# Kernel tuning notes

Measured on AMD Instinct MI355X. Metric: run time of the kernel, lower is better.

The kernel has to match this reference:

```python
import jax, jax.numpy as jnp
import numpy as np

NEG_SLOPE = 0.01  # torch F.leaky_relu default


def _mlp_block(x, mask, W, b):
    # x: [B,P,V,F]; mask: [B,P,V] bool; W: [H,F]; b: [H]
    h = jax.nn.leaky_relu(jnp.einsum('bpvf,hf->bpvh', x, W) + b, NEG_SLOPE)
    m = mask[..., None]
    out = jnp.where(m, h, 0.0)                                   # zeros at masked-out slots
    neg = jnp.where(m, out, -jnp.inf)
    pool = jnp.max(neg, axis=2, keepdims=True)                   # [B,P,1,H] masked max-pool
    any_valid = jnp.any(mask, axis=2)[:, :, None, None]
    pool = jnp.where(any_valid, pool, 0.0)                       # fully-masked polylines -> 0
    rep = jnp.broadcast_to(pool, out.shape)
    return jnp.concatenate([out, rep], axis=-1)                  # [B,P,V,2H]


def setup_inputs() -> dict:
    key = jax.random.key(0)
    ks = jax.random.split(key, 8)
    B, P, V, F, H = 32, 512, 32, 16, 64
    input_var = jax.random.normal(ks[0], (B, P, V, F), dtype=jnp.float32)
    input_mask = jax.random.bernoulli(ks[1], 0.8, (B, P, V))
    s = 1.0 / np.sqrt(F)
    W1 = jax.random.uniform(ks[2], (H, F), jnp.float32, -s, s)
    b1 = jax.random.uniform(ks[3], (H,), jnp.float32, -s, s)
    s2 = 1.0 / np.sqrt(2 * H)
    W2 = jax.random.uniform(ks[4], (H, 2 * H), jnp.float32, -s2, s2)
    b2 = jax.random.uniform(ks[5], (H,), jnp.float32, -s2, s2)
    W3 = jax.random.uniform(ks[6], (H, 2 * H), jnp.float32, -s2, s2)
    b3 = jax.random.uniform(ks[7], (H,), jnp.float32, -s2, s2)
    return {"input_var": input_var, "input_mask": input_mask,
            "W1": W1, "b1": b1, "W2": W2, "b2": b2, "W3": W3, "b3": b3,
            "size1": P, "size2": V}


def reference(input_var, input_mask, W1, b1, W2, b2, W3, b3, size1, size2):
    hidden = W1.shape[0]
    x = _mlp_block(input_var, input_mask, W1, b1)
    y = _mlp_block(x, input_mask, W2, b2)
    z = _mlp_block(y, input_mask, W3, b3)
    out = z[:, :, 0, -hidden:]                                   # pooled half, same across V
    out = jnp.where(jnp.any(input_mask, axis=2)[..., None], out, 0.0)
    return out
```

## Files before the change

### kernel.cpp

```cpp
#include <hip/hip_runtime.h>
#include <math.h>

namespace {
constexpr int kXS = 72;
constexpr float kSlope = 0.01f;

typedef short bf16x8 __attribute__((ext_vector_type(8)));
typedef float f32x4  __attribute__((ext_vector_type(4)));

__device__ __forceinline__ float lrelu(float x) { return fmaxf(x, kSlope * x); }

__device__ __forceinline__ unsigned short bfrne(float a) {
    union { float f; unsigned u; } v; v.f = a;
    return (unsigned short)((v.u + 0x7FFFu + ((v.u >> 16) & 1u)) >> 16);
}

__global__ void prep_weights(const float* __restrict__ W1,
                             const float* __restrict__ W2,
                             const float* __restrict__ W3,
                             unsigned short* __restrict__ ws)
{
    int t = blockIdx.x * blockDim.x + threadIdx.x;
    if (t >= 36 * 64) return;
    int f = t >> 6, l = t & 63, c = l & 15, q = l >> 4;
    unsigned short v[8] = {0, 0, 0, 0, 0, 0, 0, 0};
    const float* src = nullptr; int row = 0, k0 = 0, K = 0;
    if (f < 4) {
        if (q < 2) { src = W1; row = 16 * f + c; k0 = q * 8; K = 16; }
    } else if (f < 20) {
        int g = f - 4;  src = W2; row = 16 * (g >> 2) + c; k0 = (g & 3) * 32 + q * 8; K = 128;
    } else {
        int g = f - 20; src = W3; row = 16 * (g >> 2) + c; k0 = (g & 3) * 32 + q * 8; K = 128;
    }
    if (src) {
        #pragma unroll
        for (int j = 0; j < 8; ++j) v[j] = bfrne(src[row * K + k0 + j]);
    }
    unsigned short* dst = ws + (size_t)f * 512 + l * 8;
    *(ushort4*)(dst)     = make_ushort4(v[0], v[1], v[2], v[3]);
    *(ushort4*)(dst + 4) = make_ushort4(v[4], v[5], v[6], v[7]);
}

__global__ __launch_bounds__(256, 4) void fused_mlp_v5(
    const float* __restrict__ X, const int* __restrict__ M,
    const unsigned short* __restrict__ WF,
    const float* __restrict__ B1, const float* __restrict__ B2,
    const float* __restrict__ B3, float* __restrict__ OUT)
{
    __shared__ __align__(16) short sX[4][2][32 * kXS];
    __shared__ __align__(16) short sP[4][2][64];

    const int t = threadIdx.x, w = t >> 6, l = t & 63, c = l & 15, q = l >> 4;
    const size_t bp = (size_t)blockIdx.x * 4 + w;

    short* xb2 = &sX[w][0][0]; short* pl2 = &sP[w][0][0];
    short* xb3 = &sX[w][1][0]; short* pl3 = &sP[w][1][0];

    float4 xr[2][2];
    if (q < 2) {
        #pragma unroll
        for (int mt = 0; mt < 2; ++mt) {
            const float4* p = (const float4*)(X + (bp * 32 + 16 * mt + c) * 16 + q * 8);
            xr[mt][0] = p[0]; xr[mt][1] = p[1];
        }
    }
    const int4* Mp = (const int4*)(M + bp * 32);
    const int4 mr0 = Mp[q], mr1 = Mp[4 + q];
    const unsigned mbits =
        (mr0.x ? 1u : 0u)  | (mr0.y ? 2u : 0u)  | (mr0.z ? 4u : 0u)  | (mr0.w ? 8u : 0u) |
        (mr1.x ? 16u : 0u) | (mr1.y ? 32u : 0u) | (mr1.z ? 64u : 0u) | (mr1.w ? 128u : 0u);
    const bool anyv = __any(mbits != 0);

    float bias1[4], bias2[4], bias3[4];
    #pragma unroll
    for (int nt = 0; nt < 4; ++nt) {
        bias1[nt] = B1[16 * nt + c];
        bias2[nt] = B2[16 * nt + c];
        bias3[nt] = B3[16 * nt + c];
    }

    f32x4 acc[2][4];

    {
        bf16x8 a1f[2];
        #pragma unroll
        for (int mt = 0; mt < 2; ++mt) {
            bf16x8 v = {};
            if (q < 2) {
                float4 f0 = xr[mt][0], f1 = xr[mt][1];
                v[0] = (short)bfrne(f0.x); v[1] = (short)bfrne(f0.y);
                v[2] = (short)bfrne(f0.z); v[3] = (short)bfrne(f0.w);
                v[4] = (short)bfrne(f1.x); v[5] = (short)bfrne(f1.y);
                v[6] = (short)bfrne(f1.z); v[7] = (short)bfrne(f1.w);
            }
            a1f[mt] = v;
        }
        #pragma unroll
        for (int nt = 0; nt < 4; ++nt) {
            bf16x8 wf = *(const bf16x8*)(WF + (size_t)nt * 512 + l * 8);
            f32x4 c0 = { bias1[nt], bias1[nt], bias1[nt], bias1[nt] };
            acc[0][nt] = __builtin_amdgcn_mfma_f32_16x16x32_bf16(a1f[0], wf, c0, 0, 0, 0);
            acc[1][nt] = __builtin_amdgcn_mfma_f32_16x16x32_bf16(a1f[1], wf, c0, 0, 0, 0);
        }
    }

    auto epilogue = [&](short* xb, short* pl) {
        float pool[4];
        #pragma unroll
        for (int nt = 0; nt < 4; ++nt) {
            float pv = -INFINITY;
            #pragma unroll
            for (int mt = 0; mt < 2; ++mt) {
                short* base = &xb[(16 * mt + 4 * q) * kXS + 16 * nt + c];
                #pragma unroll
                for (int r = 0; r < 4; ++r) {
                    float y = lrelu(acc[mt][nt][r]);
                    bool mk = (mbits >> (mt * 4 + r)) & 1;
                    float o = mk ? y : 0.f;
                    pv = mk ? fmaxf(pv, y) : pv;
                    base[r * kXS] = (short)bfrne(o);
                }
            }
            pv = fmaxf(pv, __shfl_xor(pv, 16));
            pv = fmaxf(pv, __shfl_xor(pv, 32));
            pool[nt] = anyv ? pv : 0.f;
        }
        float ps = (q & 2) ? ((q & 1) ? pool[3] : pool[2])
                           : ((q & 1) ? pool[1] : pool[0]);
        pl[16 * q + c] = (short)bfrne(ps);
    };

    auto layerK = [&](const short* xb, const short* pl, int fb, const float (&bias)[4]) {
        bf16x8 a00 = *(const bf16x8*)&xb[(     c) * kXS      + q * 8];
        bf16x8 a01 = *(const bf16x8*)&xb[(16 + c) * kXS      + q * 8];
        bf16x8 a10 = *(const bf16x8*)&xb[(     c) * kXS + 32 + q * 8];
        bf16x8 a11 = *(const bf16x8*)&xb[(16 + c) * kXS + 32 + q * 8];
        bf16x8 ap0 = *(const bf16x8*)&pl[q * 8];
        bf16x8 ap1 = *(const bf16x8*)&pl[32 + q * 8];
        #pragma unroll
        for (int nt = 0; nt < 4; ++nt) {
            acc[0][nt] = f32x4{ bias[nt], bias[nt], bias[nt], bias[nt] };
            acc[1][nt] = acc[0][nt];
        }
        #pragma unroll
        for (int ks = 0; ks < 4; ++ks) {
            bf16x8 am0 = (ks == 0) ? a00 : (ks == 1) ? a10 : (ks == 2) ? ap0 : ap1;
            bf16x8 am1 = (ks == 0) ? a01 : (ks == 1) ? a11 : (ks == 2) ? ap0 : ap1;
            #pragma unroll
            for (int nt = 0; nt < 4; ++nt) {
                bf16x8 wf = *(const bf16x8*)(WF + ((size_t)(fb + nt * 4 + ks)) * 512 + l * 8);
                acc[0][nt] = __builtin_amdgcn_mfma_f32_16x16x32_bf16(am0, wf, acc[0][nt], 0, 0, 0);
                acc[1][nt] = __builtin_amdgcn_mfma_f32_16x16x32_bf16(am1, wf, acc[1][nt], 0, 0, 0);
            }
        }
    };

    epilogue(xb2, pl2);
    layerK(xb2, pl2, 4, bias2);
    epilogue(xb3, pl3);
    layerK(xb3, pl3, 20, bias3);

    {
        float pool[4];
        #pragma unroll
        for (int nt = 0; nt < 4; ++nt) {
            float pv = -INFINITY;
            #pragma unroll
            for (int mt = 0; mt < 2; ++mt)
                #pragma unroll
                for (int r = 0; r < 4; ++r) {
                    bool mk = (mbits >> (mt * 4 + r)) & 1;
                    float y = lrelu(acc[mt][nt][r]);
                    pv = mk ? fmaxf(pv, y) : pv;
                }
            pv = fmaxf(pv, __shfl_xor(pv, 16));
            pv = fmaxf(pv, __shfl_xor(pv, 32));
            pool[nt] = anyv ? pv : 0.f;
        }
        float ps = (q & 2) ? ((q & 1) ? pool[3] : pool[2])
                           : ((q & 1) ? pool[1] : pool[0]);
        OUT[bp * 64 + 16 * q + c] = ps;
    }
}
}

extern "C" void kernel_launch(void* const* d_in, const int* in_sizes, int n_in,
                              void* d_out, int out_size, void* d_ws, size_t ws_size,
                              hipStream_t stream) {
    (void)in_sizes; (void)n_in; (void)ws_size; (void)out_size;
    const float* X  = (const float*)d_in[0];
    const int*   M  = (const int*)d_in[1];
    const float* W1 = (const float*)d_in[2];
    const float* B1 = (const float*)d_in[3];
    const float* W2 = (const float*)d_in[4];
    const float* B2 = (const float*)d_in[5];
    const float* W3 = (const float*)d_in[6];
    const float* B3 = (const float*)d_in[7];
    float* OUT = (float*)d_out;
    unsigned short* WF = (unsigned short*)d_ws;

    prep_weights<<<(36 * 64 + 255) / 256, 256, 0, stream>>>(W1, W2, W3, WF);
    fused_mlp_v5<<<4096, 256, 0, stream>>>(X, M, WF, B1, B2, B3, OUT);
}
```

Measured before the change: 116.6 us.

## Rewrite fused MLP with fp16 32x32 MFMA, packed-half epilogue, and prepacked mask

Replaces the bf16 16x16x32 MFMA path with fp16 32x32x16 MFMA, and each wave now handles two polylines. The epilogue applies bias after the matmul and does leaky-relu and masked max-pool with packed half-precision instructions, using additive -inf mask offsets. Activations go to shared memory in a swizzled byte layout and are regathered with perm. A prep kernel packs the mask into bitfields and converts the weights to fp16. The goal is fewer instructions per element and better MFMA efficiency, at the cost of fp16 rounding in the epilogue and lower occupancy (launch bounds 3).

```diff
diff --git a/kernel.cpp b/kernel.cpp
--- a/kernel.cpp
+++ b/kernel.cpp
@@ -2,185 +2,195 @@
 #include <math.h>
 
 namespace {
-constexpr int kXS = 72;
-constexpr float kSlope = 0.01f;
-
-typedef short bf16x8 __attribute__((ext_vector_type(8)));
-typedef float f32x4  __attribute__((ext_vector_type(4)));
-
-__device__ __forceinline__ float lrelu(float x) { return fmaxf(x, kSlope * x); }
-
-__device__ __forceinline__ unsigned short bfrne(float a) {
-    union { float f; unsigned u; } v; v.f = a;
-    return (unsigned short)((v.u + 0x7FFFu + ((v.u >> 16) & 1u)) >> 16);
-}
-
-__global__ void prep_weights(const float* __restrict__ W1,
-                             const float* __restrict__ W2,
-                             const float* __restrict__ W3,
-                             unsigned short* __restrict__ ws)
+
+typedef _Float16 f16x8 __attribute__((ext_vector_type(8)));
+typedef _Float16 f16x2 __attribute__((ext_vector_type(2)));
+typedef float    f32x16 __attribute__((ext_vector_type(16)));
+typedef unsigned int uint;
+
+__device__ __forceinline__ uint pkrtz(float a, float b) {
+    return __builtin_bit_cast(uint, __builtin_amdgcn_cvt_pkrtz(a, b));
+}
+__device__ __forceinline__ uint pk_add(uint a, uint b) {
+    uint r; asm("v_pk_add_f16 %0, %1, %2" : "=v"(r) : "v"(a), "v"(b)); return r;
+}
+__device__ __forceinline__ uint pk_mul(uint a, uint b) {
+    uint r; asm("v_pk_mul_f16 %0, %1, %2" : "=v"(r) : "v"(a), "v"(b)); return r;
+}
+__device__ __forceinline__ uint pk_max(uint a, uint b) {
+    uint r; asm("v_pk_max_f16 %0, %1, %2" : "=v"(r) : "v"(a), "v"(b)); return r;
+}
+
+__global__ void prep_pack(const float* __restrict__ W1, const float* __restrict__ W2,
+                          const float* __restrict__ W3, const int* __restrict__ M,
+                          unsigned short* __restrict__ wsW, uint* __restrict__ wsM)
 {
     int t = blockIdx.x * blockDim.x + threadIdx.x;
-    if (t >= 36 * 64) return;
-    int f = t >> 6, l = t & 63, c = l & 15, q = l >> 4;
-    unsigned short v[8] = {0, 0, 0, 0, 0, 0, 0, 0};
-    const float* src = nullptr; int row = 0, k0 = 0, K = 0;
-    if (f < 4) {
-        if (q < 2) { src = W1; row = 16 * f + c; k0 = q * 8; K = 16; }
-    } else if (f < 20) {
-        int g = f - 4;  src = W2; row = 16 * (g >> 2) + c; k0 = (g & 3) * 32 + q * 8; K = 128;
-    } else {
-        int g = f - 20; src = W3; row = 16 * (g >> 2) + c; k0 = (g & 3) * 32 + q * 8; K = 128;
-    }
-    if (src) {
-        #pragma unroll
-        for (int j = 0; j < 8; ++j) v[j] = bfrne(src[row * K + k0 + j]);
-    }
-    unsigned short* dst = ws + (size_t)f * 512 + l * 8;
-    *(ushort4*)(dst)     = make_ushort4(v[0], v[1], v[2], v[3]);
-    *(ushort4*)(dst + 4) = make_ushort4(v[4], v[5], v[6], v[7]);
-}
-
-__global__ __launch_bounds__(256, 4) void fused_mlp_v5(
-    const float* __restrict__ X, const int* __restrict__ M,
+    if (t < 34 * 64) {
+        int f = t >> 6, l = t & 63, nb = l & 31, kg = l >> 5;
+        const float* src; int K, ki, nt2;
+        if (f < 2)       { src = W1; K = 16;  ki = 0;           nt2 = f; }
+        else if (f < 18) { int g = f - 2;  src = W2; K = 128; ki = g >> 1; nt2 = g & 1; }
+        else             { int g = f - 18; src = W3; K = 128; ki = g >> 1; nt2 = g & 1; }
+        const float* s = src + (size_t)(32 * nt2 + nb) * K + 16 * ki + 8 * kg;
+        uint4 q;
+        q.x = pkrtz(s[0], s[1]); q.y = pkrtz(s[2], s[3]);
+        q.z = pkrtz(s[4], s[5]); q.w = pkrtz(s[6], s[7]);
+        *(uint4*)(wsW + (size_t)f * 512 + l * 8) = q;
+    } else if (t < 34 * 64 + 16384) {
+        int bp = t - 34 * 64;
+        const int4* mp = (const int4*)(M + bp * 32);
+        uint bits = 0;
+        #pragma unroll
+        for (int i = 0; i < 8; ++i) {
+            int4 v = mp[i];
+            bits |= ((v.x ? 1u : 0u) | (v.y ? 2u : 0u) |
+                     (v.z ? 4u : 0u) | (v.w ? 8u : 0u)) << (4 * i);
+        }
+        wsM[bp] = bits;
+    }
+}
+
+__global__ __launch_bounds__(256, 3) void fused_mlp_v10(
+    const float* __restrict__ X, const uint* __restrict__ MPK,
     const unsigned short* __restrict__ WF,
     const float* __restrict__ B1, const float* __restrict__ B2,
     const float* __restrict__ B3, float* __restrict__ OUT)
 {
-    __shared__ __align__(16) short sX[4][2][32 * kXS];
-    __shared__ __align__(16) short sP[4][2][64];
-
-    const int t = threadIdx.x, w = t >> 6, l = t & 63, c = l & 15, q = l >> 4;
-    const size_t bp = (size_t)blockIdx.x * 4 + w;
-
-    short* xb2 = &sX[w][0][0]; short* pl2 = &sP[w][0][0];
-    short* xb3 = &sX[w][1][0]; short* pl3 = &sP[w][1][0];
-
-    float4 xr[2][2];
-    if (q < 2) {
-        #pragma unroll
-        for (int mt = 0; mt < 2; ++mt) {
-            const float4* p = (const float4*)(X + (bp * 32 + 16 * mt + c) * 16 + q * 8);
-            xr[mt][0] = p[0]; xr[mt][1] = p[1];
-        }
-    }
-    const int4* Mp = (const int4*)(M + bp * 32);
-    const int4 mr0 = Mp[q], mr1 = Mp[4 + q];
-    const unsigned mbits =
-        (mr0.x ? 1u : 0u)  | (mr0.y ? 2u : 0u)  | (mr0.z ? 4u : 0u)  | (mr0.w ? 8u : 0u) |
-        (mr1.x ? 16u : 0u) | (mr1.y ? 32u : 0u) | (mr1.z ? 64u : 0u) | (mr1.w ? 128u : 0u);
-    const bool anyv = __any(mbits != 0);
-
-    float bias1[4], bias2[4], bias3[4];
+    __shared__ __align__(16) unsigned char sXb[4][2][4096];
+    __shared__ __align__(16) _Float16 sP[4][2][64];
+
+    const int t = threadIdx.x, w = t >> 6, l = t & 63;
+    const int hb = l >> 5, mtl = (l >> 4) & 1;
+    const size_t bp0 = (size_t)blockIdx.x * 8 + w * 2;
+
+    unsigned char* sb[2] = { &sXb[w][0][0], &sXb[w][1][0] };
+    _Float16*     pl[2] = { &sP[w][0][0],  &sP[w][1][0]  };
+
+    uint wb0 = (uint)((l & 7) * 32 + mtl * 256 + ((l >> 3) & 1) * 1024 + hb * 8);
+    wb0 ^= (uint)(mtl << 5);
+    const uint wb1 = (wb0 + 512u) ^ 64u;
+    const uint rb = (uint)(mtl * 2048 + hb * 1024 + ((l & 15) >> 1) * 4);
+    const uint sel = (l & 1) ? 0x07060302u : 0x05040100u;
+    const uint SL2 = pkrtz(0.01f, 0.01f);
+
+    bool anyv[2]; uint adm[2][4][2];
     #pragma unroll
-    for (int nt = 0; nt < 4; ++nt) {
-        bias1[nt] = B1[16 * nt + c];
-        bias2[nt] = B2[16 * nt + c];
-        bias3[nt] = B3[16 * nt + c];
-    }
-
-    f32x4 acc[2][4];
+    for (int u = 0; u < 2; ++u) {
+        uint mk = MPK[bp0 + u];
+        anyv[u] = (mk != 0u);
+        #pragma unroll
+        for (int g = 0; g < 4; ++g) {
+            uint nib = (mk >> (8 * g + 4 * hb)) & 15u;
+            adm[u][g][0] = (nib & 1u ? 0u : 0xFC00u) | (nib & 2u ? 0u : 0xFC000000u);
+            adm[u][g][1] = (nib & 4u ? 0u : 0xFC00u) | (nib & 8u ? 0u : 0xFC000000u);
+        }
+    }
+
+    f16x8 a1f[2];
+    #pragma unroll
+    for (int u = 0; u < 2; ++u) {
+        const float4* xp = (const float4*)(X + ((bp0 + u) * 32 + (l & 31)) * 16 + 8 * hb);
+        float4 x0 = xp[0], x1 = xp[1];
+        uint4 q;
+        q.x = pkrtz(x0.x, x0.y); q.y = pkrtz(x0.z, x0.w);
+        q.z = pkrtz(x1.x, x1.y); q.w = pkrtz(x1.z, x1.w);
+        a1f[u] = __builtin_bit_cast(f16x8, q);
+    }
+
+    f32x16 zc;
+    #pragma unroll
+    for (int i = 0; i < 16; ++i) zc[i] = 0.f;
+
+    f32x16 acc[2][2];
 
     {
-        bf16x8 a1f[2];
-        #pragma unroll
-        for (int mt = 0; mt < 2; ++mt) {
-            bf16x8 v = {};
-            if (q < 2) {
-                float4 f0 = xr[mt][0], f1 = xr[mt][1];
-                v[0] = (short)bfrne(f0.x); v[1] = (short)bfrne(f0.y);
-                v[2] = (short)bfrne(f0.z); v[3] = (short)bfrne(f0.w);
-                v[4] = (short)bfrne(f1.x); v[5] = (short)bfrne(f1.y);
-                v[6] = (short)bfrne(f1.z); v[7] = (short)bfrne(f1.w);
+        const _Float16* wp = (const _Float16*)WF + l * 8;
+        f16x8 wf0 = *(const f16x8*)wp;
+        f16x8 wf1 = *(const f16x8*)(wp + 512);
+        #pragma unroll
+        for (int u = 0; u < 2; ++u) {
+            acc[u][0] = __builtin_amdgcn_mfma_f32_32x32x16_f16(a1f[u], wf0, zc, 0, 0, 0);
+            acc[u][1] = __builtin_amdgcn_mfma_f32_32x32x16_f16(a1f[u], wf1, zc, 0, 0, 0);
+        }
+    }
+
+    auto epi = [&](int u, const float* __restrict__ Bp, bool dostore) {
+        unsigned char* sbu = sb[u];
+        _Float16* plu = pl[u];
+        #pragma unroll
+        for (int nt2 = 0; nt2 < 2; ++nt2) {
+            float bsc = Bp[32 * nt2 + (l & 31)];
+            uint bpk = pkrtz(bsc, bsc);
+            uint base = nt2 ? wb1 : wb0;
+            uint pp = 0xFC00FC00u;
+            #pragma unroll
+            for (int g = 0; g < 4; ++g) {
+                uint d01 = pkrtz(acc[u][nt2][4 * g + 0], acc[u][nt2][4 * g + 1]);
+                uint d23 = pkrtz(acc[u][nt2][4 * g + 2], acc[u][nt2][4 * g + 3]);
+                d01 = pk_add(d01, bpk);  d23 = pk_add(d23, bpk);
+                d01 = pk_max(d01, pk_mul(d01, SL2));
+                d23 = pk_max(d23, pk_mul(d23, SL2));
+                if (dostore) {
+                    uint2 st; st.x = d01; st.y = d23;
+                    *(uint2*)(sbu + base + (g >> 1) * 2048 + (g & 1) * 16) = st;
+                }
+                pp = pk_max(pp, pk_add(d01, adm[u][g][0]));
+                pp = pk_max(pp, pk_add(d23, adm[u][g][1]));
             }
-            a1f[mt] = v;
-        }
-        #pragma unroll
-        for (int nt = 0; nt < 4; ++nt) {
-            bf16x8 wf = *(const bf16x8*)(WF + (size_t)nt * 512 + l * 8);
-            f32x4 c0 = { bias1[nt], bias1[nt], bias1[nt], bias1[nt] };
-            acc[0][nt] = __builtin_amdgcn_mfma_f32_16x16x32_bf16(a1f[0], wf, c0, 0, 0, 0);
-            acc[1][nt] = __builtin_amdgcn_mfma_f32_16x16x32_bf16(a1f[1], wf, c0, 0, 0, 0);
-        }
-    }
-
-    auto epilogue = [&](short* xb, short* pl) {
-        float pool[4];
-        #pragma unroll
-        for (int nt = 0; nt < 4; ++nt) {
-            float pv = -INFINITY;
+            f16x2 ph = __builtin_bit_cast(f16x2, pp);
+            float pv = fmaxf((float)ph[0], (float)ph[1]);
+            pv = fmaxf(pv, __shfl_xor(pv, 32));
+            pv = anyv[u] ? pv : 0.f;
+            if (dostore) {
+                if (l < 32) plu[32 * nt2 + (l & 31)] = (_Float16)pv;
+            } else {
+                if (l < 32) OUT[(bp0 + u) * 64 + 32 * nt2 + (l & 31)] = pv;
+            }
+        }
+    };
+
+    auto layerK = [&](int fb) {
+        #pragma unroll
+        for (int ki = 0; ki < 8; ++ki) {
+            const _Float16* wp = (const _Float16*)WF + (size_t)(fb + 2 * ki) * 512 + l * 8;
+            f16x8 wf0 = *(const f16x8*)wp;
+            f16x8 wf1 = *(const f16x8*)(wp + 512);
             #pragma unroll
-            for (int mt = 0; mt < 2; ++mt) {
-                short* base = &xb[(16 * mt + 4 * q) * kXS + 16 * nt + c];
-                #pragma unroll
-                for (int r = 0; r < 4; ++r) {
-                    float y = lrelu(acc[mt][nt][r]);
-                    bool mk = (mbits >> (mt * 4 + r)) & 1;
-                    float o = mk ? y : 0.f;
-                    pv = mk ? fmaxf(pv, y) : pv;
-                    base[r * kXS] = (short)bfrne(o);
+            for (int u = 0; u < 2; ++u) {
+                f16x8 a;
+                if (ki < 4) {
+                    const unsigned char* p = sb[u] + rb + 256 * ki;
+                    uint F0 = *(const uint*)(p + 32 * (0 ^ ki));
+                    uint F1 = *(const uint*)(p + 32 * (1 ^ ki));
+                    uint F2 = *(const uint*)(p + 32 * (2 ^ ki));
+                    uint F3 = *(const uint*)(p + 32 * (3 ^ ki));
+                    uint F4 = *(const uint*)(p + 32 * (4 ^ ki));
+                    uint F5 = *(const uint*)(p + 32 * (5 ^ ki));
+                    uint F6 = *(const uint*)(p + 32 * (6 ^ ki));
+                    uint F7 = *(const uint*)(p + 32 * (7 ^ ki));
+                    uint4 q;
+                    q.x = __builtin_amdgcn_perm(F1, F0, sel);
+                    q.y = __builtin_amdgcn_perm(F3, F2, sel);
+                    q.z = __builtin_amdgcn_perm(F5, F4, sel);
+                    q.w = __builtin_amdgcn_perm(F7, F6, sel);
+                    a = __builtin_bit_cast(f16x8, q);
+                } else {
+                    a = *(const f16x8*)(pl[u] + 16 * (ki - 4) + 8 * hb);
                 }
+                acc[u][0] = __builtin_amdgcn_mfma_f32_32x32x16_f16(
+                    a, wf0, ki == 0 ? zc : acc[u][0], 0, 0, 0);
+                acc[u][1] = __builtin_amdgcn_mfma_f32_32x32x16_f16(
+                    a, wf1, ki == 0 ? zc : acc[u][1], 0, 0, 0);
             }
-            pv = fmaxf(pv, __shfl_xor(pv, 16));
-            pv = fmaxf(pv, __shfl_xor(pv, 32));
-            pool[nt] = anyv ? pv : 0.f;
-        }
-        float ps = (q & 2) ? ((q & 1) ? pool[3] : pool[2])
-                           : ((q & 1) ? pool[1] : pool[0]);
-        pl[16 * q + c] = (short)bfrne(ps);
+        }
     };
 
-    auto layerK = [&](const short* xb, const short* pl, int fb, const float (&bias)[4]) {
-        bf16x8 a00 = *(const bf16x8*)&xb[(     c) * kXS      + q * 8];
-        bf16x8 a01 = *(const bf16x8*)&xb[(16 + c) * kXS      + q * 8];
-        bf16x8 a10 = *(const bf16x8*)&xb[(     c) * kXS + 32 + q * 8];
-        bf16x8 a11 = *(const bf16x8*)&xb[(16 + c) * kXS + 32 + q * 8];
-        bf16x8 ap0 = *(const bf16x8*)&pl[q * 8];
-        bf16x8 ap1 = *(const bf16x8*)&pl[32 + q * 8];
-        #pragma unroll
-        for (int nt = 0; nt < 4; ++nt) {
-            acc[0][nt] = f32x4{ bias[nt], bias[nt], bias[nt], bias[nt] };
-            acc[1][nt] = acc[0][nt];
-        }
-        #pragma unroll
-        for (int ks = 0; ks < 4; ++ks) {
-            bf16x8 am0 = (ks == 0) ? a00 : (ks == 1) ? a10 : (ks == 2) ? ap0 : ap1;
-            bf16x8 am1 = (ks == 0) ? a01 : (ks == 1) ? a11 : (ks == 2) ? ap0 : ap1;
-            #pragma unroll
-            for (int nt = 0; nt < 4; ++nt) {
-                bf16x8 wf = *(const bf16x8*)(WF + ((size_t)(fb + nt * 4 + ks)) * 512 + l * 8);
-                acc[0][nt] = __builtin_amdgcn_mfma_f32_16x16x32_bf16(am0, wf, acc[0][nt], 0, 0, 0);
-                acc[1][nt] = __builtin_amdgcn_mfma_f32_16x16x32_bf16(am1, wf, acc[1][nt], 0, 0, 0);
-            }
-        }
-    };
-
-    epilogue(xb2, pl2);
-    layerK(xb2, pl2, 4, bias2);
-    epilogue(xb3, pl3);
-    layerK(xb3, pl3, 20, bias3);
-
-    {
-        float pool[4];
-        #pragma unroll
-        for (int nt = 0; nt < 4; ++nt) {
-            float pv = -INFINITY;
-            #pragma unroll
-            for (int mt = 0; mt < 2; ++mt)
-                #pragma unroll
-                for (int r = 0; r < 4; ++r) {
-                    bool mk = (mbits >> (mt * 4 + r)) & 1;
-                    float y = lrelu(acc[mt][nt][r]);
-                    pv = mk ? fmaxf(pv, y) : pv;
-                }
-            pv = fmaxf(pv, __shfl_xor(pv, 16));
-            pv = fmaxf(pv, __shfl_xor(pv, 32));
-            pool[nt] = anyv ? pv : 0.f;
-        }
-        float ps = (q & 2) ? ((q & 1) ? pool[3] : pool[2])
-                           : ((q & 1) ? pool[1] : pool[0]);
-        OUT[bp * 64 + 16 * q + c] = ps;
-    }
+    epi(0, B1, true);  epi(1, B1, true);
+    layerK(2);
+    epi(0, B2, true);  epi(1, B2, true);
+    layerK(18);
+    epi(0, B3, false); epi(1, B3, false);
 }
 }
 
@@ -197,8 +207,10 @@
     const float* W3 = (const float*)d_in[6];
     const float* B3 = (const float*)d_in[7];
     float* OUT = (float*)d_out;
-    unsigned short* WF = (unsigned short*)d_ws;
-
-    prep_weights<<<(36 * 64 + 255) / 256, 256, 0, stream>>>(W1, W2, W3, WF);
-    fused_mlp_v5<<<4096, 256, 0, stream>>>(X, M, WF, B1, B2, B3, OUT);
-}
+
+    unsigned short* WF  = (unsigned short*)d_ws;
+    uint*           MPK = (uint*)((char*)d_ws + 34816);
+
+    prep_pack<<<(34 * 64 + 16384 + 255) / 256, 256, 0, stream>>>(W1, W2, W3, M, WF, MPK);
+    fused_mlp_v10<<<2048, 256, 0, stream>>>(X, MPK, WF, B1, B2, B3, OUT);
+}
```

Measured after the change: 114.8 us. Within noise of the previous version (-1.6%).
